# Optimization experiments

Measured on AMD Instinct MI355X. Metric: run time of the kernel, lower is better.

Reference implementation:

```python
import jax, jax.numpy as jnp
import numpy as np

ORDER = 2  # diffusion steps per support
NUM_LAYERS = 2


def gconv(z, supports, W, b):
    # z: [B,N,C]; supports: [S,N,N]; concat [z, S1 z, S1^2 z, S2 z, S2^2 z] -> dense proj
    feats = [z]
    for si in range(supports.shape[0]):
        s = supports[si]
        zk = z
        for _ in range(ORDER):
            zk = jnp.einsum('mn,bnc->bmc', s, zk)
            feats.append(zk)
    zcat = jnp.concatenate(feats, axis=-1)  # [B,N,C*(1+S*ORDER)]
    return zcat @ W + b


def dcgru_cell(x, h, supports, Wg, bg, Wc, bc):
    H = h.shape[-1]
    zr = jax.nn.sigmoid(gconv(jnp.concatenate([x, h], axis=-1), supports, Wg, bg))
    z, r = zr[..., :H], zr[..., H:]
    hc = jnp.tanh(gconv(jnp.concatenate([x, r * h], axis=-1), supports, Wc, bc))
    return z * h + (1.0 - z) * hc


def setup_inputs() -> dict:
    key = jax.random.key(0)
    ks = jax.random.split(key, 32)
    B, T, N, D_IN, H = 64, 12, 325, 2, 128
    K = 1 + 2 * ORDER  # 5 diffusion matrices
    inp = {}
    inp['source'] = jax.random.normal(ks[0], (B, T, N, D_IN), jnp.float32)
    inp['targets'] = jax.random.normal(ks[1], (B, T, N, D_IN), jnp.float32)
    u = jax.random.uniform(ks[2], (2, N, N), jnp.float32)
    inp['supports'] = u / jnp.sum(u, axis=-1, keepdims=True)  # row-stochastic random walks
    sc = 0.05
    inp['enc_Wg0'] = sc * jax.random.normal(ks[3], ((D_IN + H) * K, 2 * H), jnp.float32)
    inp['enc_bg0'] = jnp.zeros((2 * H,), jnp.float32)
    inp['enc_Wc0'] = sc * jax.random.normal(ks[4], ((D_IN + H) * K, H), jnp.float32)
    inp['enc_bc0'] = jnp.zeros((H,), jnp.float32)
    inp['enc_Wg1'] = sc * jax.random.normal(ks[5], ((H + H) * K, 2 * H), jnp.float32)
    inp['enc_bg1'] = jnp.zeros((2 * H,), jnp.float32)
    inp['enc_Wc1'] = sc * jax.random.normal(ks[6], ((H + H) * K, H), jnp.float32)
    inp['enc_bc1'] = jnp.zeros((H,), jnp.float32)
    inp['dec_Wg0'] = sc * jax.random.normal(ks[7], ((D_IN + H) * K, 2 * H), jnp.float32)
    inp['dec_bg0'] = jnp.zeros((2 * H,), jnp.float32)
    inp['dec_Wc0'] = sc * jax.random.normal(ks[8], ((D_IN + H) * K, H), jnp.float32)
    inp['dec_bc0'] = jnp.zeros((H,), jnp.float32)
    inp['dec_Wg1'] = sc * jax.random.normal(ks[9], ((H + H) * K, 2 * H), jnp.float32)
    inp['dec_bg1'] = jnp.zeros((2 * H,), jnp.float32)
    inp['dec_Wc1'] = sc * jax.random.normal(ks[10], ((H + H) * K, H), jnp.float32)
    inp['dec_bc1'] = jnp.zeros((H,), jnp.float32)
    inp['Wp'] = sc * jax.random.normal(ks[11], (H, D_IN), jnp.float32)
    inp['bp'] = jnp.zeros((D_IN,), jnp.float32)
    return inp


def _forward(source, targets, supports,
             enc_Wg0, enc_bg0, enc_Wc0, enc_bc0, enc_Wg1, enc_bg1, enc_Wc1, enc_bc1,
             dec_Wg0, dec_bg0, dec_Wc0, dec_bc0, dec_Wg1, dec_bg1, dec_Wc1, dec_bc1,
             Wp, bp):
    B, T_in, N, D_in = source.shape
    T_out = targets.shape[1]
    enc_params = [(enc_Wg0, enc_bg0, enc_Wc0, enc_bc0), (enc_Wg1, enc_bg1, enc_Wc1, enc_bc1)]
    dec_params = [(dec_Wg0, dec_bg0, dec_Wc0, dec_bc0), (dec_Wg1, dec_bg1, dec_Wc1, dec_bc1)]

    # ---- encoder: per layer, scan over time ----
    cur = jnp.swapaxes(source, 0, 1)  # [T,B,N,C]
    enc_finals = []
    for (Wg, bg, Wc, bc) in enc_params:
        H = Wc.shape[-1]
        h0 = jnp.zeros((B, N, H), source.dtype)
        def step(h, xt, Wg=Wg, bg=bg, Wc=Wc, bc=bc):
            h2 = dcgru_cell(xt, h, supports, Wg, bg, Wc, bc)
            return h2, h2
        hT, hs = jax.lax.scan(step, h0, cur)
        enc_finals.append(hT)
        cur = hs

    # ---- decoder (teacher_forcing_ratio = 0 for determinism) ----
    out_dim = Wp.shape[-1]
    go = jnp.zeros((B, N, out_dim), source.dtype)  # GO symbol

    def dec_step(carry, _):
        states, cur_in = carry
        new_states = []
        x = cur_in
        for i, (Wg, bg, Wc, bc) in enumerate(dec_params):
            s = dcgru_cell(x, states[i], supports, Wg, bg, Wc, bc)
            x = s
            new_states.append(s)
        out = jnp.einsum('bnh,ho->bno', x, Wp) + bp  # [B,N,out_dim]
        return (tuple(new_states), out), out

    _, outs = jax.lax.scan(dec_step, (tuple(enc_finals), go), None, length=T_out)
    return jnp.swapaxes(outs, 0, 1)  # [B,T_out,N,out_dim]


def reference(source, targets, supports,
              enc_Wg0, enc_bg0, enc_Wc0, enc_bc0, enc_Wg1, enc_bg1, enc_Wc1, enc_bc1,
              dec_Wg0, dec_bg0, dec_Wc0, dec_bc0, dec_Wg1, dec_bg1, dec_Wc1, dec_bc1,
              Wp, bp):
    return _forward(source, targets, supports,
                    enc_Wg0, enc_bg0, enc_Wc0, enc_bc0, enc_Wg1, enc_bg1, enc_Wc1, enc_bc1,
                    dec_Wg0, dec_bg0, dec_Wc0, dec_bc0, dec_Wg1, dec_bg1, dec_Wc1, dec_bc1,
                    Wp, bp)
```

## Files before the change

### kernel.cpp

```cpp
#include <hip/hip_runtime.h>
#include <hip/hip_bf16.h>

#define B_  64
#define T_  12
#define N_  325
#define DIN 2
#define H_  128
#define BN  (B_*N_)
#define DPITCH 384
#define AROWS 384

typedef __hip_bfloat16 bf16;
typedef unsigned short u16;
typedef __attribute__((ext_vector_type(8))) short short8;
typedef __attribute__((ext_vector_type(4))) float f32x4;

__device__ __forceinline__ float b2f(bf16 v){ return __bfloat162float(v); }
__device__ __forceinline__ u16 f2b(float f){
    __hip_bfloat16 h = __float2bfloat16(f);
    return *reinterpret_cast<u16*>(&h);
}
__device__ __forceinline__ float ldf(const void* p, size_t i, int bf){
    return bf ? b2f(((const bf16*)p)[i]) : ((const float*)p)[i];
}

__device__ __forceinline__ void gl_lds16(const u16* g, u16* l){
    __builtin_amdgcn_global_load_lds(
        (const __attribute__((address_space(1))) unsigned int*)g,
        (__attribute__((address_space(3))) unsigned int*)l, 16, 0, 0);
}

struct FillCfg { u16 *F, *Ft; const float *x, *h; long xbs; int C, KC, Cpad, Din, b0, nb; };
struct DiffCfg { u16* F; const u16* Ft; int C, KC, Cpad, coff, ctiles, T, nb; };
struct GemmCfg { const u16* Fb; const u16* Wt; const float* bias; float* zr; float* hb;
                 int KC, KCpad, rows, gy, ct, nb; };
struct RhCfg  { u16 *F, *Ft; const float *zr, *h; int KC, Cpad, Din, b0, total, nb; };

__global__ void sniff(const void* __restrict__ sup, int* __restrict__ flag){
    if (threadIdx.x == 0 && blockIdx.x == 0){
        float sb = 0.f, sf = 0.f;
        for (int n = 0; n < N_; ++n){
            sb += b2f(((const bf16*)sup)[n]);
            sf += ((const float*)sup)[n];
        }
        float db = fabsf(sb - 1.f), df = fabsf(sf - 1.f);
        *flag = (db < df) ? 1 : 0;
    }
}

struct CvtArgs { const void* src[12]; float* dst[12]; int n[12]; };

__global__ void cvt_all(CvtArgs a, const int* __restrict__ flag){
    int ii = blockIdx.y;
    int i  = blockIdx.x*256 + threadIdx.x;
    if (i >= a.n[ii]) return;
    a.dst[ii][i] = ldf(a.src[ii], i, *flag);
}

__global__ void support_prep(const void* __restrict__ sup, const int* __restrict__ flag,
                             float* __restrict__ msq){
    int bf = *flag;
    int s = blockIdx.z;
    int m = blockIdx.y*16 + threadIdx.y;
    int n = blockIdx.x*16 + threadIdx.x;
    __shared__ float As[16][17], Bs[16][17];
    size_t base = (size_t)s*N_*N_;
    float acc = 0.f;
    for (int j0 = 0; j0 < N_; j0 += 16){
        As[threadIdx.y][threadIdx.x] = (m < N_ && j0+threadIdx.x < N_) ? ldf(sup, base + (size_t)m*N_ + j0+threadIdx.x, bf) : 0.f;
        Bs[threadIdx.y][threadIdx.x] = (j0+threadIdx.y < N_ && n < N_) ? ldf(sup, base + (size_t)(j0+threadIdx.y)*N_ + n, bf) : 0.f;
        __syncthreads();
        #pragma unroll
        for (int jj=0; jj<16; ++jj) acc += As[threadIdx.y][jj]*Bs[jj][threadIdx.x];
        __syncthreads();
    }
    if (m < N_ && n < N_){
        msq[(size_t)(2*s  )*N_*N_ + m*N_ + n] = ldf(sup, base + (size_t)m*N_ + n, bf);
        msq[(size_t)(2*s+1)*N_*N_ + m*N_ + n] = acc;
    }
}

__global__ void asq_prep(const float* __restrict__ msq, u16* __restrict__ asq){
    int idx = blockIdx.x*256 + threadIdx.x;
    int total = 4*AROWS*DPITCH;
    if (idx >= total) return;
    int col = idx % DPITCH;
    int rm  = idx / DPITCH;
    int m   = rm % AROWS;
    int k   = rm / AROWS;
    asq[idx] = (m < N_ && col < N_) ? f2b(msq[((size_t)k*N_ + m)*N_ + col]) : 0;
}

__global__ __launch_bounds__(256) void wtrans(const void* __restrict__ W, u16* __restrict__ Wt,
                                              int KC, int Nout, int KCpad,
                                              const int* __restrict__ flag){
    int bf = *flag;
    int k0 = blockIdx.x*64, c0 = blockIdx.y*64;
    int tid = threadIdx.x;
    __shared__ u16 T[64][72];
    #pragma unroll
    for (int it=0; it<2; ++it){
        int lin = it*256 + tid;
        int kl = lin >> 3, seg = lin & 7;
        int gk = k0 + kl, gc = c0 + seg*8;
        u16 tmp[8];
        #pragma unroll
        for (int e=0;e<8;++e) tmp[e] = (gk < KC) ? f2b(ldf(W, (size_t)gk*Nout + gc + e, bf)) : 0;
        *(uint4*)&T[kl][seg*8] = *(const uint4*)tmp;
    }
    __syncthreads();
    #pragma unroll
    for (int it=0; it<2; ++it){
        int lin = it*256 + tid;
        int cl = lin >> 3, seg = lin & 7;
        u16 tmp[8];
        #pragma unroll
        for (int j=0;j<8;++j) tmp[j] = T[seg*8+j][cl];
        *(uint4*)(Wt + (size_t)(c0+cl)*KCpad + k0 + seg*8) = *(const uint4*)tmp;
    }
}

__global__ __launch_bounds__(256) void fill_k(FillCfg ca, FillCfg cb, int na){
    int bi = blockIdx.x;
    FillCfg c = ca;
    if (bi >= na){ c = cb; bi -= na; }
    int gyc  = c.Cpad >> 6;
    int nblk = bi % 6;
    int rest = bi / 6;
    int cblk = rest % gyc;
    int bl   = rest / gyc;
    int bg = c.b0 + bl;
    int n0 = nblk*64, c0 = cblk*64;
    int tid = threadIdx.x;
    __shared__ u16 T[64][72];
    #pragma unroll
    for (int it=0; it<2; ++it){
        int lin = it*256 + tid;
        int nl = lin >> 3, seg = lin & 7;
        int gn = n0 + nl;
        u16 tmp[8];
        #pragma unroll
        for (int e=0;e<8;++e){
            int cc = c0 + seg*8 + e;
            float v = 0.f;
            if (gn < N_ && cc < c.C)
                v = (cc < c.Din) ? c.x[(size_t)bg*c.xbs + (size_t)gn*c.Din + cc]
                                 : c.h[((size_t)bg*N_ + gn)*H_ + (cc - c.Din)];
            tmp[e] = f2b(v);
        }
        *(uint4*)&T[nl][seg*8] = *(const uint4*)tmp;
        if (gn < N_){
            int cbase = c0 + seg*8;
            u16* dst = c.F + ((size_t)bl*N_ + gn)*c.KC + cbase;
            if (cbase + 7 < c.C){
                *(uint4*)dst = *(const uint4*)tmp;
            } else {
                #pragma unroll
                for (int e=0;e<8;++e) if (cbase + e < c.C) dst[e] = tmp[e];
            }
        }
    }
    __syncthreads();
    #pragma unroll
    for (int it=0; it<2; ++it){
        int lin = it*256 + tid;
        int cl = lin >> 3, seg = lin & 7;
        u16 tmp[8];
        #pragma unroll
        for (int j=0;j<8;++j) tmp[j] = T[seg*8+j][cl];
        *(uint4*)(c.Ft + (size_t)bl*c.Cpad*DPITCH + (size_t)(c0+cl)*DPITCH + n0 + seg*8)
            = *(const uint4*)tmp;
    }
}

__global__ void rh_k(RhCfg ca, RhCfg cb, int na){
    int blk = blockIdx.x;
    RhCfg c = ca;
    if (blk >= na){ c = cb; blk -= na; }
    int idx = blk*256 + threadIdx.x;
    if (idx >= c.total) return;
    int j   = idx & 127;
    int bnl = idx >> 7;
    int bl  = bnl / N_;
    int n   = bnl % N_;
    float r  = c.zr[(size_t)bnl*256 + 128 + j];
    float hv = c.h[((size_t)c.b0*N_ + bnl)*128 + j];
    u16 v = f2b(r * hv);
    c.F[(size_t)bnl*c.KC + c.Din + j] = v;
    c.Ft[((size_t)bl*c.Cpad + c.Din + j)*DPITCH + n] = v;
}

__global__ __launch_bounds__(256) void diffuse_k(DiffCfg ca, DiffCfg cb, int na,
                                                 const u16* __restrict__ asq){
    int bi = blockIdx.x;
    DiffCfg c = ca;
    if (bi >= na){ c = cb; bi -= na; }
    int xcd = bi & 7, m8 = bi >> 3;
    int tg = m8 / 12, s = m8 % 12;
    int t = tg*8 + xcd;
    if (t >= c.T) return;
    int bl = t / c.ctiles, cbk = t % c.ctiles;
    int y = s % 3, k = s / 3;

    const u16* A    = asq + (size_t)k*AROWS*DPITCH;
    const u16* Bt_g = c.Ft + ((size_t)bl*c.Cpad + c.coff)*DPITCH;
    u16*       Cm   = c.F + (size_t)bl*N_*c.KC + (size_t)(k+1)*c.C + c.coff;

    int m0 = y * 128;
    int c0 = cbk * 64;
    int tid = threadIdx.x;
    int wv = tid >> 6, lane = tid & 63, l15 = lane & 15, quad = lane >> 4;
    int lr = lane >> 3, ls = lane & 7;

    __shared__ u16 As[128*64];
    __shared__ u16 Bs[64*64];

    f32x4 acc[2][4];
    #pragma unroll
    for (int i2=0;i2<2;++i2)
        #pragma unroll
        for (int j=0;j<4;++j) acc[i2][j] = (f32x4){0.f,0.f,0.f,0.f};

    for (int k0 = 0; k0 < N_; k0 += 64){
        #pragma unroll
        for (int j=0;j<4;++j){
            int row = wv*32 + j*8 + lr;
            int seg = ls ^ lr;
            gl_lds16(A + (size_t)(m0+row)*DPITCH + k0 + seg*8, &As[(wv*32 + j*8)*64]);
        }
        #pragma unroll
        for (int j=0;j<2;++j){
            int row = wv*16 + j*8 + lr;
            int seg = ls ^ lr;
            gl_lds16(Bt_g + (size_t)(c0+row)*DPITCH + k0 + seg*8, &Bs[(wv*16 + j*8)*64]);
        }
        __syncthreads();
        #pragma unroll
        for (int ks = 0; ks < 64; ks += 32){
            int sw = (((ks>>3) + quad) ^ (l15 & 7)) << 3;
            short8 a0 = *(const short8*)&As[(wv*32      + l15)*64 + sw];
            short8 a1 = *(const short8*)&As[(wv*32 + 16 + l15)*64 + sw];
            short8 b0 = *(const short8*)&Bs[(     l15)*64 + sw];
            short8 b1 = *(const short8*)&Bs[(16 + l15)*64 + sw];
            short8 b2 = *(const short8*)&Bs[(32 + l15)*64 + sw];
            short8 b3 = *(const short8*)&Bs[(48 + l15)*64 + sw];
            acc[0][0] = __builtin_amdgcn_mfma_f32_16x16x32_bf16(a0,b0,acc[0][0],0,0,0);
            acc[0][1] = __builtin_amdgcn_mfma_f32_16x16x32_bf16(a0,b1,acc[0][1],0,0,0);
            acc[0][2] = __builtin_amdgcn_mfma_f32_16x16x32_bf16(a0,b2,acc[0][2],0,0,0);
            acc[0][3] = __builtin_amdgcn_mfma_f32_16x16x32_bf16(a0,b3,acc[0][3],0,0,0);
            acc[1][0] = __builtin_amdgcn_mfma_f32_16x16x32_bf16(a1,b0,acc[1][0],0,0,0);
            acc[1][1] = __builtin_amdgcn_mfma_f32_16x16x32_bf16(a1,b1,acc[1][1],0,0,0);
            acc[1][2] = __builtin_amdgcn_mfma_f32_16x16x32_bf16(a1,b2,acc[1][2],0,0,0);
            acc[1][3] = __builtin_amdgcn_mfma_f32_16x16x32_bf16(a1,b3,acc[1][3],0,0,0);
        }
        __syncthreads();
    }
    #pragma unroll
    for (int i2=0;i2<2;++i2){
        #pragma unroll
        for (int j=0;j<4;++j){
            int cc = c0 + j*16 + l15;
            #pragma unroll
            for (int r=0;r<4;++r){
                int m = m0 + wv*32 + i2*16 + quad*4 + r;
                if (m < N_ && c.coff + cc < c.C) Cm[(size_t)m*c.KC + cc] = f2b(acc[i2][j][r]);
            }
        }
    }
}

template<int MODE>
__global__ __launch_bounds__(256) void gemm_k(GemmCfg ca, GemmCfg cb, int na){
    int bi = blockIdx.x;
    GemmCfg c = ca;
    if (bi >= na){ c = cb; bi -= na; }
    int xcd = bi & 7, q = bi >> 3;
    int cbk = q % c.ct;
    int rt  = (q / c.ct)*8 + xcd;
    if (rt >= c.gy) return;
    int r0 = rt * 128;
    int c0 = cbk * 64;
    int tid = threadIdx.x;
    int wv = tid >> 6, lane = tid & 63, l15 = lane & 15, quad = lane >> 4;
    int lr = lane >> 3, ls = lane & 7;

    __shared__ u16 As[128*64];
    __shared__ u16 Bs[64*64];

    f32x4 acc[2][4];
    #pragma unroll
    for (int i2=0;i2<2;++i2)
        #pragma unroll
        for (int j=0;j<4;++j) acc[i2][j] = (f32x4){0.f,0.f,0.f,0.f};

    for (int k0 = 0; k0 < c.KCpad; k0 += 64){
        if (k0 + 64 <= c.KC){
            #pragma unroll
            for (int j=0;j<4;++j){
                int row = wv*32 + j*8 + lr;
                int seg = ls ^ lr;
                gl_lds16(c.Fb + (size_t)(r0+row)*c.KC + k0 + seg*8, &As[(wv*32 + j*8)*64]);
            }
        } else {
            #pragma unroll
            for (int it=0; it<4; ++it){
                int lin = it*256 + tid;
                int row = lin >> 3, sp = lin & 7;
                int seg = sp ^ (row & 7);
                int gr = r0 + row, gk = k0 + seg*8;
                u16 tmp[8];
                #pragma unroll
                for (int e=0;e<8;++e)
                    tmp[e] = (gk+e < c.KC) ? c.Fb[(size_t)gr*c.KC + gk+e] : (u16)0;
                *(uint4*)&As[row*64 + sp*8] = *(const uint4*)tmp;
            }
        }
        #pragma unroll
        for (int j=0;j<2;++j){
            int row = wv*16 + j*8 + lr;
            int seg = ls ^ lr;
            gl_lds16(c.Wt + (size_t)(c0+row)*c.KCpad + k0 + seg*8, &Bs[(wv*16 + j*8)*64]);
        }
        __syncthreads();
        #pragma unroll
        for (int ks = 0; ks < 64; ks += 32){
            int sw = (((ks>>3) + quad) ^ (l15 & 7)) << 3;
            short8 a0 = *(const short8*)&As[(wv*32      + l15)*64 + sw];
            short8 a1 = *(const short8*)&As[(wv*32 + 16 + l15)*64 + sw];
            short8 b0 = *(const short8*)&Bs[(     l15)*64 + sw];
            short8 b1 = *(const short8*)&Bs[(16 + l15)*64 + sw];
            short8 b2 = *(const short8*)&Bs[(32 + l15)*64 + sw];
            short8 b3 = *(const short8*)&Bs[(48 + l15)*64 + sw];
            acc[0][0] = __builtin_amdgcn_mfma_f32_16x16x32_bf16(a0,b0,acc[0][0],0,0,0);
            acc[0][1] = __builtin_amdgcn_mfma_f32_16x16x32_bf16(a0,b1,acc[0][1],0,0,0);
            acc[0][2] = __builtin_amdgcn_mfma_f32_16x16x32_bf16(a0,b2,acc[0][2],0,0,0);
            acc[0][3] = __builtin_amdgcn_mfma_f32_16x16x32_bf16(a0,b3,acc[0][3],0,0,0);
            acc[1][0] = __builtin_amdgcn_mfma_f32_16x16x32_bf16(a1,b0,acc[1][0],0,0,0);
            acc[1][1] = __builtin_amdgcn_mfma_f32_16x16x32_bf16(a1,b1,acc[1][1],0,0,0);
            acc[1][2] = __builtin_amdgcn_mfma_f32_16x16x32_bf16(a1,b2,acc[1][2],0,0,0);
            acc[1][3] = __builtin_amdgcn_mfma_f32_16x16x32_bf16(a1,b3,acc[1][3],0,0,0);
        }
        __syncthreads();
    }
    #pragma unroll
    for (int i2=0;i2<2;++i2){
        #pragma unroll
        for (int j=0;j<4;++j){
            int cc = c0 + j*16 + l15;
            #pragma unroll
            for (int r=0;r<4;++r){
                int gr = r0 + wv*32 + i2*16 + quad*4 + r;
                if (gr >= c.rows) continue;
                float v = acc[i2][j][r] + c.bias[cc];
                if (MODE == 0){
                    v = 1.f/(1.f + __expf(-v));
                    c.zr[(size_t)gr*256 + cc] = v;
                } else {
                    float hc   = tanhf(v);
                    float z    = c.zr[(size_t)gr*256 + cc];
                    float hold = c.hb[(size_t)gr*128 + cc];
                    c.hb[(size_t)gr*128 + cc] = z*hold + (1.f - z)*hc;
                }
            }
        }
    }
}

__global__ __launch_bounds__(256) void proj(const float* __restrict__ h1,
                                            const float* __restrict__ Wp,
                                            const float* __restrict__ bp,
                                            float* __restrict__ xdec,
                                            float* __restrict__ out, int t){
    int row  = blockIdx.x * 4 + (threadIdx.x >> 6);
    int lane = threadIdx.x & 63;
    float v0 = h1[(size_t)row*128 + lane];
    float v1 = h1[(size_t)row*128 + 64 + lane];
    float w00 = Wp[lane*2+0],      w01 = Wp[lane*2+1];
    float w10 = Wp[(64+lane)*2+0], w11 = Wp[(64+lane)*2+1];
    float a0 = v0*w00 + v1*w10;
    float a1 = v0*w01 + v1*w11;
    #pragma unroll
    for (int off=32; off>0; off>>=1){
        a0 += __shfl_down(a0, off);
        a1 += __shfl_down(a1, off);
    }
    if (lane == 0){
        a0 += bp[0];
        a1 += bp[1];
        xdec[(size_t)row*2+0] = a0;
        xdec[(size_t)row*2+1] = a1;
        int b = row / N_, n = row % N_;
        size_t o = ((size_t)(b*T_ + t)*N_ + n)*2;
        out[o]   = a0;
        out[o+1] = a1;
    }
}

struct Layer {
    u16 *F, *Ft; float *zr; float *h;
    const u16 *Wg, *Wc; const float *bg, *bc;
    int C, KC, KCpad, Din, ctiles, Cpad;
};

extern "C" void kernel_launch(void* const* d_in, const int* in_sizes, int n_in,
                              void* d_out, int out_size, void* d_ws, size_t ws_size,
                              hipStream_t stream){
    float* out = (float*)d_out;

    char* pb = (char*)d_ws;
    auto alloc = [&](size_t bytes)->void*{
        void* r = (void*)pb;
        pb += (bytes + 255) & ~(size_t)255;
        return r;
    };

    int* flag = (int*)alloc(16);
    sniff<<<1, 64, 0, stream>>>(d_in[2], flag);

    const int idxs[11] = {0,4,6,8,10,12,14,16,18,19,20};
    float* cw[21] = {nullptr};
    CvtArgs ca;
    int maxn = 0;
    for (int ii = 0; ii < 11; ++ii){
        int i = idxs[ii];
        int n = in_sizes[i];
        cw[i] = (float*)alloc((size_t)n*4);
        ca.src[ii] = d_in[i];
        ca.dst[ii] = cw[i];
        ca.n[ii]   = n;
        if (n > maxn) maxn = n;
    }
    cvt_all<<<dim3((maxn+255)/256, 11), 256, 0, stream>>>(ca, flag);
    const float* src = cw[0];

    float* msq  = (float*)alloc((size_t)4*N_*N_*4);
    float* h0   = (float*)alloc((size_t)BN*H_*4);
    float* h1   = (float*)alloc((size_t)BN*H_*4);
    float* xdec = (float*)alloc((size_t)BN*DIN*4);
    u16*   asq  = (u16*)alloc((size_t)4*AROWS*DPITCH*2);

    const int widx[8]  = {3,5,7,9,11,13,15,17};
    const int wKC[8]   = {650,650,1280,1280,650,650,1280,1280};
    const int wNout[8] = {256,128,256,128,256,128,256,128};
    u16* wt[8];
    for (int i=0;i<8;++i){
        int KCpad = (wKC[i] + 63) & ~63;
        wt[i] = (u16*)alloc((size_t)wNout[i]*KCpad*2);
        wtrans<<<dim3(KCpad/64, wNout[i]/64), 256, 0, stream>>>(d_in[widx[i]], wt[i], wKC[i], wNout[i], KCpad, flag);
    }

    {
        dim3 g((N_+15)/16, (N_+15)/16, 2), b(16,16);
        support_prep<<<g, b, 0, stream>>>(d_in[2], flag, msq);
        int tot = 4*AROWS*DPITCH;
        asq_prep<<<dim3((tot+255)/256), 256, 0, stream>>>(msq, asq);
    }
    hipMemsetAsync(h0, 0, sizeof(float)*(size_t)BN*H_*2, stream);

    size_t fixed = (size_t)(pb - (char*)d_ws);
    size_t need0 = (size_t)BN*256*4 + (size_t)BN*650*2  + (size_t)B_*192*DPITCH*2;
    size_t need1 = (size_t)BN*256*4 + (size_t)BN*1280*2 + (size_t)B_*256*DPITCH*2;
    bool dual = (fixed + need0 + need1 + (4<<20)) <= ws_size;

    auto mkFill = [&](Layer& L, const float* x, long xbs, int b0, int Bc)->FillCfg{
        return FillCfg{L.F, L.Ft, x, L.h, xbs, L.C, L.KC, L.Cpad, L.Din, b0,
                       6*(L.Cpad/64)*Bc};
    };
    auto mkD1 = [&](Layer& L, int Bc)->DiffCfg{
        int T = Bc*L.ctiles;
        return DiffCfg{L.F, L.Ft, L.C, L.KC, L.Cpad, 0, L.ctiles, T, 12*(((T+7)/8)*8)};
    };
    auto mkD2 = [&](Layer& L, int Bc)->DiffCfg{
        int T = Bc*2;
        return DiffCfg{L.F, L.Ft, L.C, L.KC, L.Cpad, L.Din, 2, T, 12*(((T+7)/8)*8)};
    };
    auto mkG0 = [&](Layer& L, int b0, int Bc)->GemmCfg{
        int rows = Bc*N_, gy = (rows+127)/128;
        return GemmCfg{L.F, L.Wg, L.bg, L.zr, L.h + (size_t)b0*N_*H_,
                       L.KC, L.KCpad, rows, gy, 4, 8*((gy+7)/8)*4};
    };
    auto mkG1 = [&](Layer& L, int b0, int Bc)->GemmCfg{
        int rows = Bc*N_, gy = (rows+127)/128;
        return GemmCfg{L.F, L.Wc, L.bc, L.zr, L.h + (size_t)b0*N_*H_,
                       L.KC, L.KCpad, rows, gy, 2, 8*((gy+7)/8)*2};
    };
    auto mkRh = [&](Layer& L, int b0, int Bc)->RhCfg{
        int total = Bc*N_*H_;
        return RhCfg{L.F, L.Ft, L.zr, L.h, L.KC, L.Cpad, L.Din, b0, total, (total+255)/256};
    };
    auto runCellSeq = [&](Layer& L, const float* x, long xbs, int b0, int Bc){
        FillCfg f = mkFill(L, x, xbs, b0, Bc);
        fill_k<<<dim3(f.nb), 256, 0, stream>>>(f, f, f.nb);
        DiffCfg d1 = mkD1(L, Bc);
        diffuse_k<<<dim3(d1.nb), 256, 0, stream>>>(d1, d1, d1.nb, asq);
        GemmCfg g0 = mkG0(L, b0, Bc);
        gemm_k<0><<<dim3(g0.nb), 256, 0, stream>>>(g0, g0, g0.nb);
        RhCfg r = mkRh(L, b0, Bc);
        rh_k<<<dim3(r.nb), 256, 0, stream>>>(r, r, r.nb);
        DiffCfg d2 = mkD2(L, Bc);
        diffuse_k<<<dim3(d2.nb), 256, 0, stream>>>(d2, d2, d2.nb, asq);
        GemmCfg g1 = mkG1(L, b0, Bc);
        gemm_k<1><<<dim3(g1.nb), 256, 0, stream>>>(g1, g1, g1.nb);
    };

    if (dual){
        float* zr0 = (float*)alloc((size_t)BN*256*4);
        u16*   F0  = (u16*)alloc((size_t)BN*650*2);
        u16*   Ft0 = (u16*)alloc((size_t)B_*192*DPITCH*2);
        float* zr1 = (float*)alloc((size_t)BN*256*4);
        u16*   F1  = (u16*)alloc((size_t)BN*1280*2);
        u16*   Ft1 = (u16*)alloc((size_t)B_*256*DPITCH*2);
        alloc(1<<19);

        Layer E0{F0, Ft0, zr0, h0, wt[0], wt[1], cw[4],  cw[6],  130, 650, 704, 2,   3, 192};
        Layer E1{F1, Ft1, zr1, h1, wt[2], wt[3], cw[8],  cw[10], 256, 1280,1280,128, 4, 256};
        Layer D0{F0, Ft0, zr0, h0, wt[4], wt[5], cw[12], cw[14], 130, 650, 704, 2,   3, 192};
        Layer D1{F1, Ft1, zr1, h1, wt[6], wt[7], cw[16], cw[18], 256, 1280,1280,128, 4, 256};

        for (int s = 0; s <= T_; ++s){
            bool has0 = (s < T_), has1 = (s >= 1);
            const float* x0 = src + (size_t)s*N_*DIN;
            FillCfg f0 = mkFill(E0, x0, (long)T_*N_*DIN, 0, B_);
            FillCfg f1 = mkFill(E1, h0, (long)N_*H_,     0, B_);
            if (has0 && has1) fill_k<<<dim3(f0.nb+f1.nb),256,0,stream>>>(f0, f1, f0.nb);
            else if (has0)    fill_k<<<dim3(f0.nb),256,0,stream>>>(f0, f0, f0.nb);
            else              fill_k<<<dim3(f1.nb),256,0,stream>>>(f1, f1, f1.nb);

            DiffCfg a1 = mkD1(E0, B_), b1 = mkD1(E1, B_);
            if (has0 && has1) diffuse_k<<<dim3(a1.nb+b1.nb),256,0,stream>>>(a1, b1, a1.nb, asq);
            else if (has0)    diffuse_k<<<dim3(a1.nb),256,0,stream>>>(a1, a1, a1.nb, asq);
            else              diffuse_k<<<dim3(b1.nb),256,0,stream>>>(b1, b1, b1.nb, asq);

            GemmCfg ga = mkG0(E0, 0, B_), gb = mkG0(E1, 0, B_);
            if (has0 && has1) gemm_k<0><<<dim3(ga.nb+gb.nb),256,0,stream>>>(ga, gb, ga.nb);
            else if (has0)    gemm_k<0><<<dim3(ga.nb),256,0,stream>>>(ga, ga, ga.nb);
            else              gemm_k<0><<<dim3(gb.nb),256,0,stream>>>(gb, gb, gb.nb);

            RhCfg ra = mkRh(E0, 0, B_), rb = mkRh(E1, 0, B_);
            if (has0 && has1) rh_k<<<dim3(ra.nb+rb.nb),256,0,stream>>>(ra, rb, ra.nb);
            else if (has0)    rh_k<<<dim3(ra.nb),256,0,stream>>>(ra, ra, ra.nb);
            else              rh_k<<<dim3(rb.nb),256,0,stream>>>(rb, rb, rb.nb);

            DiffCfg a2 = mkD2(E0, B_), b2 = mkD2(E1, B_);
            if (has0 && has1) diffuse_k<<<dim3(a2.nb+b2.nb),256,0,stream>>>(a2, b2, a2.nb, asq);
            else if (has0)    diffuse_k<<<dim3(a2.nb),256,0,stream>>>(a2, a2, a2.nb, asq);
            else              diffuse_k<<<dim3(b2.nb),256,0,stream>>>(b2, b2, b2.nb, asq);

            GemmCfg ha = mkG1(E0, 0, B_), hb = mkG1(E1, 0, B_);
            if (has0 && has1) gemm_k<1><<<dim3(ha.nb+hb.nb),256,0,stream>>>(ha, hb, ha.nb);
            else if (has0)    gemm_k<1><<<dim3(ha.nb),256,0,stream>>>(ha, ha, ha.nb);
            else              gemm_k<1><<<dim3(hb.nb),256,0,stream>>>(hb, hb, hb.nb);
        }

        hipMemsetAsync(xdec, 0, sizeof(float)*(size_t)BN*DIN, stream);
        for (int t = 0; t < T_; ++t){
            runCellSeq(D0, xdec, (long)N_*DIN, 0, B_);
            runCellSeq(D1, h0,   (long)N_*H_,  0, B_);
            proj<<<dim3(BN/4), 256, 0, stream>>>(h1, cw[19], cw[20], xdec, out, t);
        }
    } else {
        size_t perb = (size_t)N_*1280*2 + (size_t)N_*256*4 + (size_t)256*DPITCH*2;
        int Bc = 64;
        while (Bc > 2 && fixed + (1<<20) + (size_t)Bc*perb > ws_size) Bc >>= 1;
        float* zr = (float*)alloc((size_t)Bc*N_*256*4);
        u16*   F  = (u16*)alloc((size_t)Bc*N_*1280*2);
        u16*   Ft = (u16*)alloc((size_t)Bc*256*DPITCH*2);
        alloc(1<<19);

        Layer SE0{F, Ft, zr, h0, wt[0], wt[1], cw[4],  cw[6],  130, 650, 704, 2,   3, 192};
        Layer SE1{F, Ft, zr, h1, wt[2], wt[3], cw[8],  cw[10], 256, 1280,1280,128, 4, 256};
        Layer SD0{F, Ft, zr, h0, wt[4], wt[5], cw[12], cw[14], 130, 650, 704, 2,   3, 192};
        Layer SD1{F, Ft, zr, h1, wt[6], wt[7], cw[16], cw[18], 256, 1280,1280,128, 4, 256};

        for (int t = 0; t < T_; ++t){
            for (int b0 = 0; b0 < B_; b0 += Bc)
                runCellSeq(SE0, src + (size_t)t*N_*DIN, (long)T_*N_*DIN, b0, Bc);
            for (int b0 = 0; b0 < B_; b0 += Bc)
                runCellSeq(SE1, h0, (long)N_*H_, b0, Bc);
        }
        hipMemsetAsync(xdec, 0, sizeof(float)*(size_t)BN*DIN, stream);
        for (int t = 0; t < T_; ++t){
            for (int b0 = 0; b0 < B_; b0 += Bc)
                runCellSeq(SD0, xdec, (long)N_*DIN, b0, Bc);
            for (int b0 = 0; b0 < B_; b0 += Bc)
                runCellSeq(SD1, h0, (long)N_*H_, b0, Bc);
            proj<<<dim3(BN/4), 256, 0, stream>>>(h1, cw[19], cw[20], xdec, out, t);
        }
    }
}
```

Measured before the change: 6.053 ms.

## Enlarge diffusion and gate GEMM tiles and pack transposed features densely

The diffusion kernel now uses 128x128 output tiles over a flattened batch-by-channel column space. Layer-0 features are packed with a pitch of 130 instead of 192, so padded columns are no longer computed or stored and tiles can span batch boundaries. The gate GEMM (mode 0) moves to 128x128 tiles with a 2x2 wave layout, and the fill kernel skips padded channel blocks. This aims to raise MFMA work per LDS load and cut wasted padding work, at the cost of more accumulator registers and a per-column batch index division in the epilogue.

```diff
diff --git a/kernel.cpp b/kernel.cpp
--- a/kernel.cpp
+++ b/kernel.cpp
@@ -31,7 +31,7 @@
 }
 
 struct FillCfg { u16 *F, *Ft; const float *x, *h; long xbs; int C, KC, Cpad, Din, b0, nb; };
-struct DiffCfg { u16* F; const u16* Ft; int C, KC, Cpad, coff, ctiles, T, nb; };
+struct DiffCfg { u16* F; const u16* Ft; int C, KC, Cpad, coff0, cstep, T, fcmax, nb; };
 struct GemmCfg { const u16* Fb; const u16* Wt; const float* bias; float* zr; float* hb;
                  int KC, KCpad, rows, gy, ct, nb; };
 struct RhCfg  { u16 *F, *Ft; const float *zr, *h; int KC, Cpad, Din, b0, total, nb; };
@@ -124,7 +124,7 @@
     int bi = blockIdx.x;
     FillCfg c = ca;
     if (bi >= na){ c = cb; bi -= na; }
-    int gyc  = c.Cpad >> 6;
+    int gyc  = (c.C + 63) >> 6;
     int nblk = bi % 6;
     int rest = bi / 6;
     int cblk = rest % gyc;
@@ -165,11 +165,13 @@
     for (int it=0; it<2; ++it){
         int lin = it*256 + tid;
         int cl = lin >> 3, seg = lin & 7;
-        u16 tmp[8];
-        #pragma unroll
-        for (int j=0;j<8;++j) tmp[j] = T[seg*8+j][cl];
-        *(uint4*)(c.Ft + (size_t)bl*c.Cpad*DPITCH + (size_t)(c0+cl)*DPITCH + n0 + seg*8)
-            = *(const uint4*)tmp;
+        if (c0 + cl < c.C){
+            u16 tmp[8];
+            #pragma unroll
+            for (int j=0;j<8;++j) tmp[j] = T[seg*8+j][cl];
+            *(uint4*)(c.Ft + ((size_t)bl*c.Cpad + (size_t)(c0+cl))*DPITCH + n0 + seg*8)
+                = *(const uint4*)tmp;
+        }
     }
 }
 
@@ -199,71 +201,72 @@
     int tg = m8 / 12, s = m8 % 12;
     int t = tg*8 + xcd;
     if (t >= c.T) return;
-    int bl = t / c.ctiles, cbk = t % c.ctiles;
     int y = s % 3, k = s / 3;
+    int fc0 = c.coff0 + t*c.cstep;
 
     const u16* A    = asq + (size_t)k*AROWS*DPITCH;
-    const u16* Bt_g = c.Ft + ((size_t)bl*c.Cpad + c.coff)*DPITCH;
-    u16*       Cm   = c.F + (size_t)bl*N_*c.KC + (size_t)(k+1)*c.C + c.coff;
+    const u16* Bt_g = c.Ft + (size_t)fc0*DPITCH;
 
     int m0 = y * 128;
-    int c0 = cbk * 64;
     int tid = threadIdx.x;
     int wv = tid >> 6, lane = tid & 63, l15 = lane & 15, quad = lane >> 4;
     int lr = lane >> 3, ls = lane & 7;
+    int wm = wv >> 1, wcx = wv & 1;
 
     __shared__ u16 As[128*64];
-    __shared__ u16 Bs[64*64];
-
-    f32x4 acc[2][4];
-    #pragma unroll
-    for (int i2=0;i2<2;++i2)
-        #pragma unroll
-        for (int j=0;j<4;++j) acc[i2][j] = (f32x4){0.f,0.f,0.f,0.f};
+    __shared__ u16 Bs[128*64];
+
+    f32x4 acc[4][4];
+    #pragma unroll
+    for (int i=0;i<4;++i)
+        #pragma unroll
+        for (int j=0;j<4;++j) acc[i][j] = (f32x4){0.f,0.f,0.f,0.f};
 
     for (int k0 = 0; k0 < N_; k0 += 64){
         #pragma unroll
         for (int j=0;j<4;++j){
-            int row = wv*32 + j*8 + lr;
+            int rbase = wv*32 + j*8;
+            int row = rbase + lr;
             int seg = ls ^ lr;
-            gl_lds16(A + (size_t)(m0+row)*DPITCH + k0 + seg*8, &As[(wv*32 + j*8)*64]);
-        }
-        #pragma unroll
-        for (int j=0;j<2;++j){
-            int row = wv*16 + j*8 + lr;
-            int seg = ls ^ lr;
-            gl_lds16(Bt_g + (size_t)(c0+row)*DPITCH + k0 + seg*8, &Bs[(wv*16 + j*8)*64]);
+            gl_lds16(A    + (size_t)(m0+row)*DPITCH + k0 + seg*8, &As[rbase*64]);
+            gl_lds16(Bt_g + (size_t)row     *DPITCH + k0 + seg*8, &Bs[rbase*64]);
         }
         __syncthreads();
         #pragma unroll
         for (int ks = 0; ks < 64; ks += 32){
             int sw = (((ks>>3) + quad) ^ (l15 & 7)) << 3;
-            short8 a0 = *(const short8*)&As[(wv*32      + l15)*64 + sw];
-            short8 a1 = *(const short8*)&As[(wv*32 + 16 + l15)*64 + sw];
-            short8 b0 = *(const short8*)&Bs[(     l15)*64 + sw];
-            short8 b1 = *(const short8*)&Bs[(16 + l15)*64 + sw];
-            short8 b2 = *(const short8*)&Bs[(32 + l15)*64 + sw];
-            short8 b3 = *(const short8*)&Bs[(48 + l15)*64 + sw];
-            acc[0][0] = __builtin_amdgcn_mfma_f32_16x16x32_bf16(a0,b0,acc[0][0],0,0,0);
-            acc[0][1] = __builtin_amdgcn_mfma_f32_16x16x32_bf16(a0,b1,acc[0][1],0,0,0);
-            acc[0][2] = __builtin_amdgcn_mfma_f32_16x16x32_bf16(a0,b2,acc[0][2],0,0,0);
-            acc[0][3] = __builtin_amdgcn_mfma_f32_16x16x32_bf16(a0,b3,acc[0][3],0,0,0);
-            acc[1][0] = __builtin_amdgcn_mfma_f32_16x16x32_bf16(a1,b0,acc[1][0],0,0,0);
-            acc[1][1] = __builtin_amdgcn_mfma_f32_16x16x32_bf16(a1,b1,acc[1][1],0,0,0);
-            acc[1][2] = __builtin_amdgcn_mfma_f32_16x16x32_bf16(a1,b2,acc[1][2],0,0,0);
-            acc[1][3] = __builtin_amdgcn_mfma_f32_16x16x32_bf16(a1,b3,acc[1][3],0,0,0);
+            short8 a[4]; short8 b[4];
+            #pragma unroll
+            for (int i=0;i<4;++i) a[i] = *(const short8*)&As[(wm*64 + i*16 + l15)*64 + sw];
+            #pragma unroll
+            for (int j=0;j<4;++j) b[j] = *(const short8*)&Bs[(wcx*64 + j*16 + l15)*64 + sw];
+            #pragma unroll
+            for (int i=0;i<4;++i)
+                #pragma unroll
+                for (int j=0;j<4;++j)
+                    acc[i][j] = __builtin_amdgcn_mfma_f32_16x16x32_bf16(a[i],b[j],acc[i][j],0,0,0);
         }
         __syncthreads();
     }
-    #pragma unroll
-    for (int i2=0;i2<2;++i2){
+    int blj[4], ccj[4], okj[4];
+    #pragma unroll
+    for (int j=0;j<4;++j){
+        int fc = fc0 + wcx*64 + j*16 + l15;
+        int bl = fc / c.Cpad;
+        blj[j] = bl;
+        ccj[j] = fc - bl*c.Cpad;
+        okj[j] = (fc < c.fcmax);
+    }
+    #pragma unroll
+    for (int i=0;i<4;++i){
         #pragma unroll
         for (int j=0;j<4;++j){
-            int cc = c0 + j*16 + l15;
+            if (!okj[j]) continue;
+            u16* Cm = c.F + (size_t)blj[j]*N_*c.KC + (size_t)(k+1)*c.C + ccj[j];
             #pragma unroll
             for (int r=0;r<4;++r){
-                int m = m0 + wv*32 + i2*16 + quad*4 + r;
-                if (m < N_ && c.coff + cc < c.C) Cm[(size_t)m*c.KC + cc] = f2b(acc[i2][j][r]);
+                int m = m0 + wm*64 + i*16 + quad*4 + r;
+                if (m < N_) Cm[(size_t)m*c.KC] = f2b(acc[i][j][r]);
             }
         }
     }
@@ -271,6 +274,8 @@
 
 template<int MODE>
 __global__ __launch_bounds__(256) void gemm_k(GemmCfg ca, GemmCfg cb, int na){
+    constexpr int CB = (MODE==0) ? 128 : 64;
+    constexpr int MI = (MODE==0) ? 4 : 2;
     int bi = blockIdx.x;
     GemmCfg c = ca;
     if (bi >= na){ c = cb; bi -= na; }
@@ -279,27 +284,30 @@
     int rt  = (q / c.ct)*8 + xcd;
     if (rt >= c.gy) return;
     int r0 = rt * 128;
-    int c0 = cbk * 64;
+    int c0 = cbk * CB;
     int tid = threadIdx.x;
     int wv = tid >> 6, lane = tid & 63, l15 = lane & 15, quad = lane >> 4;
     int lr = lane >> 3, ls = lane & 7;
+    int wm  = (MODE==0) ? (wv >> 1) : wv;
+    int wcx = (MODE==0) ? (wv & 1)  : 0;
 
     __shared__ u16 As[128*64];
-    __shared__ u16 Bs[64*64];
-
-    f32x4 acc[2][4];
-    #pragma unroll
-    for (int i2=0;i2<2;++i2)
-        #pragma unroll
-        for (int j=0;j<4;++j) acc[i2][j] = (f32x4){0.f,0.f,0.f,0.f};
+    __shared__ u16 Bs[CB*64];
+
+    f32x4 acc[MI][4];
+    #pragma unroll
+    for (int i=0;i<MI;++i)
+        #pragma unroll
+        for (int j=0;j<4;++j) acc[i][j] = (f32x4){0.f,0.f,0.f,0.f};
 
     for (int k0 = 0; k0 < c.KCpad; k0 += 64){
         if (k0 + 64 <= c.KC){
             #pragma unroll
             for (int j=0;j<4;++j){
-                int row = wv*32 + j*8 + lr;
+                int rbase = wv*32 + j*8;
+                int row = rbase + lr;
                 int seg = ls ^ lr;
-                gl_lds16(c.Fb + (size_t)(r0+row)*c.KC + k0 + seg*8, &As[(wv*32 + j*8)*64]);
+                gl_lds16(c.Fb + (size_t)(r0+row)*c.KC + k0 + seg*8, &As[rbase*64]);
             }
         } else {
             #pragma unroll
@@ -316,42 +324,39 @@
             }
         }
         #pragma unroll
-        for (int j=0;j<2;++j){
-            int row = wv*16 + j*8 + lr;
+        for (int j=0;j<CB/32;++j){
+            int rbase = wv*(CB/4) + j*8;
+            int row = rbase + lr;
             int seg = ls ^ lr;
-            gl_lds16(c.Wt + (size_t)(c0+row)*c.KCpad + k0 + seg*8, &Bs[(wv*16 + j*8)*64]);
+            gl_lds16(c.Wt + (size_t)(c0+row)*c.KCpad + k0 + seg*8, &Bs[rbase*64]);
         }
         __syncthreads();
         #pragma unroll
         for (int ks = 0; ks < 64; ks += 32){
             int sw = (((ks>>3) + quad) ^ (l15 & 7)) << 3;
-            short8 a0 = *(const short8*)&As[(wv*32      + l15)*64 + sw];
-            short8 a1 = *(const short8*)&As[(wv*32 + 16 + l15)*64 + sw];
-            short8 b0 = *(const short8*)&Bs[(     l15)*64 + sw];
-            short8 b1 = *(const short8*)&Bs[(16 + l15)*64 + sw];
-            short8 b2 = *(const short8*)&Bs[(32 + l15)*64 + sw];
-            short8 b3 = *(const short8*)&Bs[(48 + l15)*64 + sw];
-            acc[0][0] = __builtin_amdgcn_mfma_f32_16x16x32_bf16(a0,b0,acc[0][0],0,0,0);
-            acc[0][1] = __builtin_amdgcn_mfma_f32_16x16x32_bf16(a0,b1,acc[0][1],0,0,0);
-            acc[0][2] = __builtin_amdgcn_mfma_f32_16x16x32_bf16(a0,b2,acc[0][2],0,0,0);
-            acc[0][3] = __builtin_amdgcn_mfma_f32_16x16x32_bf16(a0,b3,acc[0][3],0,0,0);
-            acc[1][0] = __builtin_amdgcn_mfma_f32_16x16x32_bf16(a1,b0,acc[1][0],0,0,0);
-            acc[1][1] = __builtin_amdgcn_mfma_f32_16x16x32_bf16(a1,b1,acc[1][1],0,0,0);
-            acc[1][2] = __builtin_amdgcn_mfma_f32_16x16x32_bf16(a1,b2,acc[1][2],0,0,0);
-            acc[1][3] = __builtin_amdgcn_mfma_f32_16x16x32_bf16(a1,b3,acc[1][3],0,0,0);
+            short8 a[MI]; short8 b[4];
+            #pragma unroll
+            for (int i=0;i<MI;++i) a[i] = *(const short8*)&As[(wm*(MI*16) + i*16 + l15)*64 + sw];
+            #pragma unroll
+            for (int j=0;j<4;++j) b[j] = *(const short8*)&Bs[(wcx*64 + j*16 + l15)*64 + sw];
+            #pragma unroll
+            for (int i=0;i<MI;++i)
+                #pragma unroll
+                for (int j=0;j<4;++j)
+                    acc[i][j] = __builtin_amdgcn_mfma_f32_16x16x32_bf16(a[i],b[j],acc[i][j],0,0,0);
         }
         __syncthreads();
     }
     #pragma unroll
-    for (int i2=0;i2<2;++i2){
-        #pragma unroll
-        for (int j=0;j<4;++j){
-            int cc = c0 + j*16 + l15;
+    for (int j=0;j<4;++j){
+        int cc = c0 + wcx*64 + j*16 + l15;
+        #pragma unroll
+        for (int i=0;i<MI;++i){
             #pragma unroll
             for (int r=0;r<4;++r){
-                int gr = r0 + wv*32 + i2*16 + quad*4 + r;
+                int gr = r0 + wm*(MI*16) + i*16 + quad*4 + r;
                 if (gr >= c.rows) continue;
-                float v = acc[i2][j][r] + c.bias[cc];
+                float v = acc[i][j][r] + c.bias[cc];
                 if (MODE == 0){
                     v = 1.f/(1.f + __expf(-v));
                     c.zr[(size_t)gr*256 + cc] = v;
@@ -399,7 +404,7 @@
 struct Layer {
     u16 *F, *Ft; float *zr; float *h;
     const u16 *Wg, *Wc; const float *bg, *bc;
-    int C, KC, KCpad, Din, ctiles, Cpad;
+    int C, KC, KCpad, Din, Cpad;
 };
 
 extern "C" void kernel_launch(void* const* d_in, const int* in_sizes, int n_in,
@@ -458,26 +463,28 @@
     hipMemsetAsync(h0, 0, sizeof(float)*(size_t)BN*H_*2, stream);
 
     size_t fixed = (size_t)(pb - (char*)d_ws);
-    size_t need0 = (size_t)BN*256*4 + (size_t)BN*650*2  + (size_t)B_*192*DPITCH*2;
+    size_t need0 = (size_t)BN*256*4 + (size_t)BN*650*2  + (size_t)B_*130*DPITCH*2;
     size_t need1 = (size_t)BN*256*4 + (size_t)BN*1280*2 + (size_t)B_*256*DPITCH*2;
     bool dual = (fixed + need0 + need1 + (4<<20)) <= ws_size;
 
     auto mkFill = [&](Layer& L, const float* x, long xbs, int b0, int Bc)->FillCfg{
         return FillCfg{L.F, L.Ft, x, L.h, xbs, L.C, L.KC, L.Cpad, L.Din, b0,
-                       6*(L.Cpad/64)*Bc};
+                       6*((L.C+63)>>6)*Bc};
     };
     auto mkD1 = [&](Layer& L, int Bc)->DiffCfg{
-        int T = Bc*L.ctiles;
-        return DiffCfg{L.F, L.Ft, L.C, L.KC, L.Cpad, 0, L.ctiles, T, 12*(((T+7)/8)*8)};
+        int fcmax = Bc*L.Cpad;
+        int T = (fcmax + 127) >> 7;
+        return DiffCfg{L.F, L.Ft, L.C, L.KC, L.Cpad, 0, 128, T, fcmax,
+                       12*(((T+7)/8)*8)};
     };
     auto mkD2 = [&](Layer& L, int Bc)->DiffCfg{
-        int T = Bc*2;
-        return DiffCfg{L.F, L.Ft, L.C, L.KC, L.Cpad, L.Din, 2, T, 12*(((T+7)/8)*8)};
+        return DiffCfg{L.F, L.Ft, L.C, L.KC, L.Cpad, L.Din, L.Cpad, Bc, Bc*L.Cpad,
+                       12*(((Bc+7)/8)*8)};
     };
     auto mkG0 = [&](Layer& L, int b0, int Bc)->GemmCfg{
         int rows = Bc*N_, gy = (rows+127)/128;
         return GemmCfg{L.F, L.Wg, L.bg, L.zr, L.h + (size_t)b0*N_*H_,
-                       L.KC, L.KCpad, rows, gy, 4, 8*((gy+7)/8)*4};
+                       L.KC, L.KCpad, rows, gy, 2, 8*((gy+7)/8)*2};
     };
     auto mkG1 = [&](Layer& L, int b0, int Bc)->GemmCfg{
         int rows = Bc*N_, gy = (rows+127)/128;
@@ -506,16 +513,16 @@
     if (dual){
         float* zr0 = (float*)alloc((size_t)BN*256*4);
         u16*   F0  = (u16*)alloc((size_t)BN*650*2);
-        u16*   Ft0 = (u16*)alloc((size_t)B_*192*DPITCH*2);
+        u16*   Ft0 = (u16*)alloc((size_t)B_*130*DPITCH*2);
         float* zr1 = (float*)alloc((size_t)BN*256*4);
         u16*   F1  = (u16*)alloc((size_t)BN*1280*2);
         u16*   Ft1 = (u16*)alloc((size_t)B_*256*DPITCH*2);
         alloc(1<<19);
 
-        Layer E0{F0, Ft0, zr0, h0, wt[0], wt[1], cw[4],  cw[6],  130, 650, 704, 2,   3, 192};
-        Layer E1{F1, Ft1, zr1, h1, wt[2], wt[3], cw[8],  cw[10], 256, 1280,1280,128, 4, 256};
-        Layer D0{F0, Ft0, zr0, h0, wt[4], wt[5], cw[12], cw[14], 130, 650, 704, 2,   3, 192};
-        Layer D1{F1, Ft1, zr1, h1, wt[6], wt[7], cw[16], cw[18], 256, 1280,1280,128, 4, 256};
+        Layer E0{F0, Ft0, zr0, h0, wt[0], wt[1], cw[4],  cw[6],  130, 650, 704, 2,   130};
+        Layer E1{F1, Ft1, zr1, h1, wt[2], wt[3], cw[8],  cw[10], 256, 1280,1280,128, 256};
+        Layer D0{F0, Ft0, zr0, h0, wt[4], wt[5], cw[12], cw[14], 130, 650, 704, 2,   130};
+        Layer D1{F1, Ft1, zr1, h1, wt[6], wt[7], cw[16], cw[18], 256, 1280,1280,128, 256};
 
         for (int s = 0; s <= T_; ++s){
             bool has0 = (s < T_), has1 = (s >= 1);
@@ -567,10 +574,10 @@
         u16*   Ft = (u16*)alloc((size_t)Bc*256*DPITCH*2);
         alloc(1<<19);
 
-        Layer SE0{F, Ft, zr, h0, wt[0], wt[1], cw[4],  cw[6],  130, 650, 704, 2,   3, 192};
-        Layer SE1{F, Ft, zr, h1, wt[2], wt[3], cw[8],  cw[10], 256, 1280,1280,128, 4, 256};
-        Layer SD0{F, Ft, zr, h0, wt[4], wt[5], cw[12], cw[14], 130, 650, 704, 2,   3, 192};
-        Layer SD1{F, Ft, zr, h1, wt[6], wt[7], cw[16], cw[18], 256, 1280,1280,128, 4, 256};
+        Layer SE0{F, Ft, zr, h0, wt[0], wt[1], cw[4],  cw[6],  130, 650, 704, 2,   130};
+        Layer SE1{F, Ft, zr, h1, wt[2], wt[3], cw[8],  cw[10], 256, 1280,1280,128, 256};
+        Layer SD0{F, Ft, zr, h0, wt[4], wt[5], cw[12], cw[14], 130, 650, 704, 2,   130};
+        Layer SD1{F, Ft, zr, h1, wt[6], wt[7], cw[16], cw[18], 256, 1280,1280,128, 256};
 
         for (int t = 0; t < T_; ++t){
             for (int b0 = 0; b0 < B_; b0 += Bc)
```

New measurement: 6.668 ms. +10.1%, slower.
